# Optimization experiments

Hardware: AMD Instinct MI355X
Metric: run time of the kernel (lower is better)

The kernel has to match this reference:

```python
import jax, jax.numpy as jnp
import numpy as np

NUM_SRC = 262144   # rows of node_mars (children)
NUM_ELS = 131072   # rows of element_mars (product nodes)
B = 256            # batch size
N0, C0 = 65536, 2  # group 0: 65536 nodes with arity 2
N1, C1 = 65536, 8  # group 1: 65536 nodes with arity 8


def setup_inputs() -> dict:
    key = jax.random.key(0)
    k1, k2, k3 = jax.random.split(key, 3)
    node_mars = jax.random.normal(k1, (NUM_SRC, B), dtype=jnp.float32)
    element_mars = jnp.zeros((NUM_ELS, B), dtype=jnp.float32)
    # disjoint destination ids per arity group
    nids0 = jnp.arange(N0, dtype=jnp.int64 if jax.config.jax_enable_x64 else jnp.int32)
    nids1 = jnp.arange(N0, N0 + N1, dtype=nids0.dtype)
    cids0 = jax.random.randint(k2, (N0, C0), 0, NUM_SRC)
    cids1 = jax.random.randint(k3, (N1, C1), 0, NUM_SRC)
    return {
        "node_mars": node_mars,
        "element_mars": element_mars,
        "nids0": nids0,
        "cids0": cids0,
        "nids1": nids1,
        "cids1": cids1,
    }


def reference(node_mars, element_mars, nids0, cids0, nids1, cids1):
    # ProdLayer.forward: for each arity group g:
    #   element_mars[nids_g] = node_mars[cids_g].sum(dim=1)
    out = element_mars
    out = out.at[nids0].set(node_mars[cids0].sum(axis=1))  # [N0,C0,B] -> [N0,B]
    out = out.at[nids1].set(node_mars[cids1].sum(axis=1))  # [N1,C1,B] -> [N1,B]
    return out
```

## Files before the change

kernel.cpp:

```cpp
#include <hip/hip_runtime.h>


template <int C>
__global__ __launch_bounds__(256) void prod_group_kernel(
    const float* __restrict__ node_mars,
    const int*   __restrict__ nids,
    const int*   __restrict__ cids,
    float*       __restrict__ out,
    int n_nodes,
    int f4_log2,
    int src_rows,
    int out_rows)
{
    const int f4_mask = (1 << f4_log2) - 1;
    const int total = n_nodes << f4_log2;
    const int stride = gridDim.x * blockDim.x;

    for (int gid = blockIdx.x * blockDim.x + threadIdx.x; gid < total; gid += stride) {
        const int node = gid >> f4_log2;
        const int c4   = gid & f4_mask;

        const int nid = nids[node];
        if ((unsigned)nid >= (unsigned)out_rows) continue;

        float4 acc = make_float4(0.f, 0.f, 0.f, 0.f);
#pragma unroll
        for (int c = 0; c < C; ++c) {
            const int cid = cids[node * C + c];
            if ((unsigned)cid < (unsigned)src_rows) {
                const float4 v = reinterpret_cast<const float4*>(
                    node_mars + ((size_t)cid << (f4_log2 + 2)))[c4];
                acc.x += v.x;
                acc.y += v.y;
                acc.z += v.z;
                acc.w += v.w;
            }
        }

        reinterpret_cast<float4*>(out + ((size_t)nid << (f4_log2 + 2)))[c4] = acc;
    }
}

extern "C" void kernel_launch(void* const* d_in, const int* in_sizes, int n_in,
                              void* d_out, int out_size, void* d_ws, size_t ws_size,
                              hipStream_t stream)
{
    const float* node_mars = (const float*)d_in[0];
    const int* nids0 = (const int*)d_in[2];
    const int* cids0 = (const int*)d_in[3];
    const int* nids1 = (const int*)d_in[4];
    const int* cids1 = (const int*)d_in[5];

    float* out = (float*)d_out;

    const int N0 = in_sizes[2];
    const int C0 = in_sizes[3] / (N0 > 0 ? N0 : 1);
    const int N1 = in_sizes[4];
    const int C1 = in_sizes[5] / (N1 > 0 ? N1 : 1);

    const int out_rows_total = N0 + N1;
    const int B = out_size / (out_rows_total > 0 ? out_rows_total : 1);
    int f4_log2 = 0;
    while ((4 << f4_log2) < B) ++f4_log2;
    const int src_rows = in_sizes[0] / (B > 0 ? B : 1);
    const int out_rows = out_size / (B > 0 ? B : 1);

    const int block = 256;
    auto grid_for = [&](long long n_nodes) {
        long long total = n_nodes << f4_log2;
        long long g = (total + block - 1) / block;
        if (g > 2048) g = 2048;
        if (g < 1) g = 1;
        return (int)g;
    };

    if (N0 > 0 && C0 == 2) {
        prod_group_kernel<2><<<grid_for(N0), block, 0, stream>>>(
            node_mars, nids0, cids0, out, N0, f4_log2, src_rows, out_rows);
    }
    if (N1 > 0 && C1 == 8) {
        prod_group_kernel<8><<<grid_for(N1), block, 0, stream>>>(
            node_mars, nids1, cids1, out, N1, f4_log2, src_rows, out_rows);
    }
}
```

Baseline: 124.8 us.

## Fuse both arity groups into one launch with nontemporal output stores

Merges the two per-group kernel launches into a single grid-stride kernel that picks the arity-2 or arity-8 path by index range. Output writes now use nontemporal stores so the write stream is kept out of cache in favour of gathered inputs. This saves one launch and the tail gap between kernels. The cost is a runtime branch per iteration and a grid capped at 2048 blocks shared by both groups, which can leave some waves mixing light and heavy work.

```diff
diff --git a/kernel.cpp b/kernel.cpp
--- a/kernel.cpp
+++ b/kernel.cpp
@@ -1,43 +1,62 @@
 #include <hip/hip_runtime.h>
 
 
+typedef float f32x4 __attribute__((ext_vector_type(4)));
+
 template <int C>
-__global__ __launch_bounds__(256) void prod_group_kernel(
+__device__ __forceinline__ void prod_one(
     const float* __restrict__ node_mars,
     const int*   __restrict__ nids,
     const int*   __restrict__ cids,
     float*       __restrict__ out,
-    int n_nodes,
+    int idx, int f4_log2, int f4_mask, int src_rows, int out_rows)
+{
+    const int node = idx >> f4_log2;
+    const int c4   = idx & f4_mask;
+
+    const int nid = nids[node];
+    if ((unsigned)nid >= (unsigned)out_rows) return;
+
+    f32x4 acc = {0.f, 0.f, 0.f, 0.f};
+#pragma unroll
+    for (int c = 0; c < C; ++c) {
+        const int cid = cids[node * C + c];
+        if ((unsigned)cid < (unsigned)src_rows) {
+            const f32x4 v = reinterpret_cast<const f32x4*>(
+                node_mars + ((size_t)cid << (f4_log2 + 2)))[c4];
+            acc += v;
+        }
+    }
+
+    __builtin_nontemporal_store(
+        acc, reinterpret_cast<f32x4*>(out + ((size_t)nid << (f4_log2 + 2))) + c4);
+}
+
+__global__ __launch_bounds__(256) void prod_fused_kernel(
+    const float* __restrict__ node_mars,
+    const int*   __restrict__ nids0,
+    const int*   __restrict__ cids0,
+    const int*   __restrict__ nids1,
+    const int*   __restrict__ cids1,
+    float*       __restrict__ out,
+    int n0, int n1,
     int f4_log2,
     int src_rows,
     int out_rows)
 {
     const int f4_mask = (1 << f4_log2) - 1;
-    const int total = n_nodes << f4_log2;
+    const int total0 = n0 << f4_log2;
+    const int total  = (n0 + n1) << f4_log2;
     const int stride = gridDim.x * blockDim.x;
 
     for (int gid = blockIdx.x * blockDim.x + threadIdx.x; gid < total; gid += stride) {
-        const int node = gid >> f4_log2;
-        const int c4   = gid & f4_mask;
-
-        const int nid = nids[node];
-        if ((unsigned)nid >= (unsigned)out_rows) continue;
-
-        float4 acc = make_float4(0.f, 0.f, 0.f, 0.f);
-#pragma unroll
-        for (int c = 0; c < C; ++c) {
-            const int cid = cids[node * C + c];
-            if ((unsigned)cid < (unsigned)src_rows) {
-                const float4 v = reinterpret_cast<const float4*>(
-                    node_mars + ((size_t)cid << (f4_log2 + 2)))[c4];
-                acc.x += v.x;
-                acc.y += v.y;
-                acc.z += v.z;
-                acc.w += v.w;
-            }
+        if (gid < total0) {
+            prod_one<2>(node_mars, nids0, cids0, out, gid,
+                        f4_log2, f4_mask, src_rows, out_rows);
+        } else {
+            prod_one<8>(node_mars, nids1, cids1, out, gid - total0,
+                        f4_log2, f4_mask, src_rows, out_rows);
         }
-
-        reinterpret_cast<float4*>(out + ((size_t)nid << (f4_log2 + 2)))[c4] = acc;
     }
 }
 
@@ -54,9 +73,7 @@
     float* out = (float*)d_out;
 
     const int N0 = in_sizes[2];
-    const int C0 = in_sizes[3] / (N0 > 0 ? N0 : 1);
     const int N1 = in_sizes[4];
-    const int C1 = in_sizes[5] / (N1 > 0 ? N1 : 1);
 
     const int out_rows_total = N0 + N1;
     const int B = out_size / (out_rows_total > 0 ? out_rows_total : 1);
@@ -66,20 +83,12 @@
     const int out_rows = out_size / (B > 0 ? B : 1);
 
     const int block = 256;
-    auto grid_for = [&](long long n_nodes) {
-        long long total = n_nodes << f4_log2;
-        long long g = (total + block - 1) / block;
-        if (g > 2048) g = 2048;
-        if (g < 1) g = 1;
-        return (int)g;
-    };
+    long long total = ((long long)N0 + N1) << f4_log2;
+    long long g = (total + block - 1) / block;
+    if (g > 2048) g = 2048;
+    if (g < 1) g = 1;
 
-    if (N0 > 0 && C0 == 2) {
-        prod_group_kernel<2><<<grid_for(N0), block, 0, stream>>>(
-            node_mars, nids0, cids0, out, N0, f4_log2, src_rows, out_rows);
-    }
-    if (N1 > 0 && C1 == 8) {
-        prod_group_kernel<8><<<grid_for(N1), block, 0, stream>>>(
-            node_mars, nids1, cids1, out, N1, f4_log2, src_rows, out_rows);
-    }
+    prod_fused_kernel<<<(int)g, block, 0, stream>>>(
+        node_mars, nids0, cids0, nids1, cids1, out,
+        N0, N1, f4_log2, src_rows, out_rows);
 }
```

After: 115.0 us. -7.8%, faster.
